# Kernel optimization log

Hardware: AMD Instinct MI355X
Metric: run time of the kernel (lower is better)

## Reference

```python
import jax, jax.numpy as jnp
import numpy as np

NEG_SLOPE = 0.2


def gat_conv(x, src, dst, W, a_src, a_dst, bias, concat, num_nodes):
    # x: [N, F_in]; W: [F_in, H*C]; a_src/a_dst: [H, C]
    H, C = a_src.shape
    h = (x @ W).reshape(num_nodes, H, C)               # [N,H,C]
    alpha_s = jnp.sum(h * a_src[None], axis=-1)        # [N,H]
    alpha_d = jnp.sum(h * a_dst[None], axis=-1)        # [N,H]
    e = jax.nn.leaky_relu(alpha_s[src] + alpha_d[dst], NEG_SLOPE)  # [E,H]
    m = jax.ops.segment_max(e, dst, num_segments=num_nodes)
    m = jnp.where(jnp.isfinite(m), m, 0.0)
    ex = jnp.exp(e - m[dst])
    denom = jax.ops.segment_sum(ex, dst, num_segments=num_nodes)
    alpha = ex / (denom[dst] + 1e-16)                  # scatter-softmax over dst
    msg = h[src] * alpha[:, :, None]                   # [E,H,C]
    out = jax.ops.segment_sum(msg, dst, num_segments=num_nodes)  # [N,H,C]
    if concat:
        out = out.reshape(num_nodes, H * C)
    else:
        out = out.mean(axis=1)
    return out + bias


def setup_inputs() -> dict:
    key = jax.random.key(0)
    ks = jax.random.split(key, 12)
    N, E = 50000, 800000
    num_concat, F_in, hid, H1, H2, n_cls = 2, 128, 64, 4, 1, 16
    x_list = jax.random.normal(ks[0], (num_concat, N, F_in), dtype=jnp.float32)
    edge_index = jax.random.randint(ks[1], (2, E), 0, N, dtype=jnp.int64)
    s = 0.1
    W1 = jax.random.normal(ks[2], (num_concat, F_in, H1 * hid), dtype=jnp.float32) * s
    att_src1 = jax.random.normal(ks[3], (num_concat, H1, hid), dtype=jnp.float32) * s
    att_dst1 = jax.random.normal(ks[4], (num_concat, H1, hid), dtype=jnp.float32) * s
    bias1 = jnp.zeros((num_concat, H1 * hid), dtype=jnp.float32)
    W2 = jax.random.normal(ks[5], (hid * H1 * num_concat, H2 * n_cls), dtype=jnp.float32) * s
    att_src2 = jax.random.normal(ks[6], (H2, n_cls), dtype=jnp.float32) * s
    att_dst2 = jax.random.normal(ks[7], (H2, n_cls), dtype=jnp.float32) * s
    bias2 = jnp.zeros((n_cls,), dtype=jnp.float32)
    return {"x_list": x_list, "edge_index": edge_index,
            "W1": W1, "att_src1": att_src1, "att_dst1": att_dst1, "bias1": bias1,
            "W2": W2, "att_src2": att_src2, "att_dst2": att_dst2, "bias2": bias2}


def reference(x_list, edge_index, W1, att_src1, att_dst1, bias1, W2, att_src2, att_dst2, bias2):
    num_concat, N, _ = x_list.shape
    loop = jnp.arange(N, dtype=edge_index.dtype)
    src = jnp.concatenate([edge_index[0], loop])  # PyG add_self_loops=True
    dst = jnp.concatenate([edge_index[1], loop])
    hidden = [jax.nn.elu(gat_conv(x_list[k], src, dst, W1[k], att_src1[k], att_dst1[k],
                                  bias1[k], True, N))
              for k in range(num_concat)]
    x = jnp.concatenate(hidden, axis=-1)           # [N, hid*H1*num_concat]
    out = gat_conv(x, src, dst, W2, att_src2, att_dst2, bias2, False, N)
    return out
```

## Files before the change

### kernel.cpp

```cpp
#include <hip/hip_runtime.h>

#define LEAKY(v) ((v) >= 0.0f ? (v) : 0.2f * (v))

typedef __attribute__((ext_vector_type(8))) short bf16x8;
typedef __attribute__((ext_vector_type(4))) float f32x4;

__device__ __forceinline__ unsigned short f2bf(float f) {
    unsigned int u = __float_as_uint(f);
    unsigned int r = u + 0x7FFFu + ((u >> 16) & 1u);
    return (unsigned short)(r >> 16);
}
__device__ __forceinline__ float bf2f(unsigned short u) {
    return __uint_as_float(((unsigned int)u) << 16);
}
__device__ __forceinline__ unsigned int pk2(float a, float b) {
    return (unsigned int)f2bf(a) | ((unsigned int)f2bf(b) << 16);
}


__global__ __launch_bounds__(256) void count_deg(const int* ei, int* deg, int E, int Etot) {
    int i = blockIdx.x * 256 + threadIdx.x;
    if (i >= Etot) return;
    int d = (i < E) ? ei[E + i] : (i - E);
    atomicAdd(&deg[d], 1);
}

__global__ __launch_bounds__(512) void scan_block(const int* deg, int* excl, int* bsum, int n) {
    __shared__ int s[512];
    int t = threadIdx.x;
    int i = blockIdx.x * 512 + t;
    int v = (i < n) ? deg[i] : 0;
    s[t] = v;
    __syncthreads();
    for (int d = 1; d < 512; d <<= 1) {
        int x = 0;
        if (t >= d) x = s[t - d];
        __syncthreads();
        if (t >= d) s[t] += x;
        __syncthreads();
    }
    if (i < n) excl[i] = s[t] - v;
    if (t == 511) bsum[blockIdx.x] = s[511];
}

__global__ __launch_bounds__(512) void scan_sums(const int* bsum, int* boff, int nb) {
    __shared__ int s[512];
    int t = threadIdx.x;
    int v = (t < nb) ? bsum[t] : 0;
    s[t] = v;
    __syncthreads();
    for (int d = 1; d < 512; d <<= 1) {
        int x = 0;
        if (t >= d) x = s[t - d];
        __syncthreads();
        if (t >= d) s[t] += x;
        __syncthreads();
    }
    boff[t] = s[t] - v;
}

__global__ __launch_bounds__(256) void finalize_off(int* csr, int* cursor, const int* boff, int n, int etot) {
    int i = blockIdx.x * 256 + threadIdx.x;
    if (i < n) {
        int v = csr[i] + boff[i >> 9];
        csr[i] = v;
        cursor[i] = v;
    }
    if (i == 0) csr[n] = etot;
}

__global__ __launch_bounds__(256) void scatter_edge(const int* ei, int* cursor, int* srcs, int* dsts,
                                                    int E, int Etot) {
    int i = blockIdx.x * 256 + threadIdx.x;
    if (i >= Etot) return;
    int s, d;
    if (i < E) { s = ei[i]; d = ei[E + i]; }
    else       { s = i - E; d = s; }
    int pos = atomicAdd(&cursor[d], 1);
    srcs[pos] = s;
    dsts[pos] = d;
}


__global__ __launch_bounds__(256) void xpack(const float* __restrict__ x, unsigned short* __restrict__ xp,
                                             int nrows) {
    int id = blockIdx.x * 256 + threadIdx.x;
    if (id >= nrows * 16) return;
    int row = id >> 4, q = id & 15;
    const float* src = x + (size_t)row * 128 + q * 8;
    float4 a = *(const float4*)src;
    float4 b = *(const float4*)(src + 4);
    uint4 v;
    v.x = pk2(a.x, a.y); v.y = pk2(a.z, a.w);
    v.z = pk2(b.x, b.y); v.w = pk2(b.z, b.w);
    *(uint4*)(xp + (size_t)row * 128 + ((q ^ (row & 7)) << 3)) = v;
}

__global__ __launch_bounds__(256) void wpack1(const float* __restrict__ W1, unsigned short* __restrict__ wt1) {
    int id = blockIdx.x * 256 + threadIdx.x;
    if (id >= 8192) return;
    int conv = id >> 12, rem = id & 4095;
    int c = rem >> 4, q = rem & 15;
    const float* src = W1 + (size_t)conv * 32768 + (size_t)(q * 8) * 256 + c;
    float w[8];
#pragma unroll
    for (int j = 0; j < 8; ++j) w[j] = src[j * 256];
    uint4 v;
    v.x = pk2(w[0], w[1]); v.y = pk2(w[2], w[3]);
    v.z = pk2(w[4], w[5]); v.w = pk2(w[6], w[7]);
    *(uint4*)(wt1 + (size_t)conv * 32768 + c * 128 + ((q ^ (c & 7)) << 3)) = v;
}

__global__ __launch_bounds__(256) void wpack2(const float* __restrict__ W2, unsigned short* __restrict__ wt2) {
    int id = blockIdx.x * 256 + threadIdx.x;
    if (id >= 1024) return;
    int s = id >> 6, l = id & 63;
    const float* src = W2 + (size_t)(s * 32 + (l >> 4) * 8) * 16 + (l & 15);
    float w[8];
#pragma unroll
    for (int j = 0; j < 8; ++j) w[j] = src[j * 16];
    uint4 v;
    v.x = pk2(w[0], w[1]); v.y = pk2(w[2], w[3]);
    v.z = pk2(w[4], w[5]); v.w = pk2(w[6], w[7]);
    *(uint4*)(wt2 + (size_t)id * 8) = v;
}


__global__ __launch_bounds__(256) void gemm1_mfma(const unsigned short* __restrict__ xp,
                                                  const unsigned short* __restrict__ wt1,
                                                  const float* __restrict__ asw, const float* __restrict__ adw,
                                                  unsigned short* __restrict__ hp,
                                                  float* __restrict__ as1, float* __restrict__ ad1, int N) {
    __shared__ unsigned short As[64 * 128];
    __shared__ unsigned short Ws[256 * 128];
    int conv = blockIdx.y;
    int t = threadIdx.x;
    int w = t >> 6, l = t & 63;

    const uint4* xsrc = (const uint4*)(xp + ((size_t)conv * N + (size_t)blockIdx.x * 64) * 128);
#pragma unroll
    for (int p = 0; p < 4; ++p) {
        int id = p * 256 + t;
        int row = id >> 4;
        int grow = blockIdx.x * 64 + row;
        uint4 v = make_uint4(0, 0, 0, 0);
        if (grow < N) v = xsrc[id];
        *(uint4*)(As + (size_t)id * 8) = v;
    }
    const uint4* wsrc = (const uint4*)(wt1 + (size_t)conv * 32768);
#pragma unroll
    for (int p = 0; p < 16; ++p) {
        int id = p * 256 + t;
        *(uint4*)(Ws + (size_t)id * 8) = wsrc[id];
    }
    __syncthreads();

    f32x4 acc[4][4];
#pragma unroll
    for (int mt = 0; mt < 4; ++mt)
#pragma unroll
        for (int nt = 0; nt < 4; ++nt) acc[mt][nt] = (f32x4){0.f, 0.f, 0.f, 0.f};

    int lr = l & 15, lg = l >> 4;
#pragma unroll
    for (int s = 0; s < 4; ++s) {
        int kq = s * 4 + lg;
        bf16x8 af[4], bf[4];
#pragma unroll
        for (int mt = 0; mt < 4; ++mt) {
            int r = mt * 16 + lr;
            af[mt] = *(const bf16x8*)(As + r * 128 + ((kq ^ (r & 7)) << 3));
        }
#pragma unroll
        for (int nt = 0; nt < 4; ++nt) {
            int c = w * 64 + nt * 16 + lr;
            bf[nt] = *(const bf16x8*)(Ws + c * 128 + ((kq ^ (c & 7)) << 3));
        }
#pragma unroll
        for (int mt = 0; mt < 4; ++mt)
#pragma unroll
            for (int nt = 0; nt < 4; ++nt)
                acc[mt][nt] = __builtin_amdgcn_mfma_f32_16x16x32_bf16(af[mt], bf[nt], acc[mt][nt], 0, 0, 0);
    }

    float aswv[4], adwv[4];
#pragma unroll
    for (int nt = 0; nt < 4; ++nt) {
        aswv[nt] = asw[conv * 256 + w * 64 + nt * 16 + lr];
        adwv[nt] = adw[conv * 256 + w * 64 + nt * 16 + lr];
    }
#pragma unroll
    for (int mt = 0; mt < 4; ++mt) {
#pragma unroll
        for (int i = 0; i < 4; ++i) {
            int grow = blockIdx.x * 64 + mt * 16 + lg * 4 + i;
            bool ok = grow < N;
            float sv = 0.f, dv = 0.f;
#pragma unroll
            for (int nt = 0; nt < 4; ++nt) {
                float hv = acc[mt][nt][i];
                if (ok) hp[(size_t)grow * 512 + (nt * 16 + lr) * 8 + conv * 4 + w] = f2bf(hv);
                sv += hv * aswv[nt];
                dv += hv * adwv[nt];
            }
#pragma unroll
            for (int o = 1; o < 16; o <<= 1) {
                sv += __shfl_xor(sv, o);
                dv += __shfl_xor(dv, o);
            }
            if (lr == 0 && ok) {
                as1[(size_t)conv * N * 4 + (size_t)grow * 4 + w] = sv;
                ad1[(size_t)conv * N * 4 + (size_t)grow * 4 + w] = dv;
            }
        }
    }
}


__global__ __launch_bounds__(256) void edge_w1(const int* __restrict__ srcs, const int* __restrict__ dsts,
                                               const float* __restrict__ as, const float* __restrict__ ad,
                                               float* __restrict__ pw, int Etot, int N4) {
    int e = blockIdx.x * 256 + threadIdx.x;
    if (e >= Etot) return;
    int s = srcs[e], d = dsts[e];
    float4 a0 = *(const float4*)(as + (size_t)s * 4);
    float4 b0 = *(const float4*)(ad + (size_t)d * 4);
    float4 a1 = *(const float4*)(as + N4 + (size_t)s * 4);
    float4 b1 = *(const float4*)(ad + N4 + (size_t)d * 4);
    float4 p0, p1;
    p0.x = __expf(LEAKY(a0.x + b0.x));
    p0.y = __expf(LEAKY(a0.y + b0.y));
    p0.z = __expf(LEAKY(a0.z + b0.z));
    p0.w = __expf(LEAKY(a0.w + b0.w));
    p1.x = __expf(LEAKY(a1.x + b1.x));
    p1.y = __expf(LEAKY(a1.y + b1.y));
    p1.z = __expf(LEAKY(a1.z + b1.z));
    p1.w = __expf(LEAKY(a1.w + b1.w));
    *(float4*)(pw + (size_t)e * 8)     = p0;
    *(float4*)(pw + (size_t)e * 8 + 4) = p1;
}


#define ACC8(g, pa, pb) {                                                      \
    float h0 = __uint_as_float((g).x << 16), h1 = __uint_as_float((g).x & 0xFFFF0000u); \
    float h2v = __uint_as_float((g).y << 16), h3 = __uint_as_float((g).y & 0xFFFF0000u); \
    float h4 = __uint_as_float((g).z << 16), h5 = __uint_as_float((g).z & 0xFFFF0000u); \
    float h6 = __uint_as_float((g).w << 16), h7 = __uint_as_float((g).w & 0xFFFF0000u); \
    den[0] += (pa).x; acc[0] += (pa).x * h0;                                   \
    den[1] += (pa).y; acc[1] += (pa).y * h1;                                   \
    den[2] += (pa).z; acc[2] += (pa).z * h2v;                                  \
    den[3] += (pa).w; acc[3] += (pa).w * h3;                                   \
    den[4] += (pb).x; acc[4] += (pb).x * h4;                                   \
    den[5] += (pb).y; acc[5] += (pb).y * h5;                                   \
    den[6] += (pb).z; acc[6] += (pb).z * h6;                                   \
    den[7] += (pb).w; acc[7] += (pb).w * h7; }

__global__ __launch_bounds__(256) void agg1_both(const unsigned short* __restrict__ hp,
                                                 const float* __restrict__ pw,
                                                 const int* __restrict__ off, const int* __restrict__ srcs,
                                                 const float* __restrict__ b1,
                                                 unsigned short* __restrict__ x2, int N) {
    int n = blockIdx.x * 4 + (threadIdx.x >> 6);
    int lane = threadIdx.x & 63;
    if (n >= N) return;
    int r0 = off[n], r1 = off[n + 1];

    float acc[8] = {0.f, 0.f, 0.f, 0.f, 0.f, 0.f, 0.f, 0.f};
    float den[8] = {0.f, 0.f, 0.f, 0.f, 0.f, 0.f, 0.f, 0.f};

    for (int base = r0; base < r1; base += 64) {
        int cnt = min(64, r1 - base);
        int my = (base + lane < r1) ? srcs[base + lane] : 0;
        int j = 0;
        for (; j + 2 <= cnt; j += 2) {
            int s0 = __shfl(my, j);
            int s1 = __shfl(my, j + 1);
            uint4 g0 = *(const uint4*)(hp + (size_t)s0 * 512 + lane * 8);
            uint4 g1 = *(const uint4*)(hp + (size_t)s1 * 512 + lane * 8);
            float4 pa0 = *(const float4*)(pw + (size_t)(base + j) * 8);
            float4 pb0 = *(const float4*)(pw + (size_t)(base + j) * 8 + 4);
            float4 pa1 = *(const float4*)(pw + (size_t)(base + j + 1) * 8);
            float4 pb1 = *(const float4*)(pw + (size_t)(base + j + 1) * 8 + 4);
            ACC8(g0, pa0, pb0);
            ACC8(g1, pa1, pb1);
        }
        if (j < cnt) {
            int s0 = __shfl(my, j);
            uint4 g0 = *(const uint4*)(hp + (size_t)s0 * 512 + lane * 8);
            float4 pa0 = *(const float4*)(pw + (size_t)(base + j) * 8);
            float4 pb0 = *(const float4*)(pw + (size_t)(base + j) * 8 + 4);
            ACC8(g0, pa0, pb0);
        }
    }

    unsigned short* xo = x2 + (size_t)n * 512;
#pragma unroll
    for (int q = 0; q < 8; ++q) {
        int k = q >> 2, hd = q & 3;
        int ofs = k * 256 + hd * 64 + lane;
        float o = acc[q] / (den[q] + 1e-16f) + b1[ofs];
        o = o > 0.f ? o : (__expf(o) - 1.0f);
        xo[ofs] = f2bf(o);
    }
}


__global__ __launch_bounds__(256) void gemm2_mfma(const unsigned short* __restrict__ x2,
                                                  const unsigned short* __restrict__ wt2,
                                                  const float* __restrict__ asw2, const float* __restrict__ adw2,
                                                  float* __restrict__ h2,
                                                  float* __restrict__ as2, float* __restrict__ ad2, int N) {
    int t = threadIdx.x;
    int w = t >> 6, l = t & 63;
    int rowbase = (blockIdx.x * 4 + w) * 16;
    if (rowbase >= N) return;
    int lr = l & 15, lg = l >> 4;

    f32x4 acc = (f32x4){0.f, 0.f, 0.f, 0.f};
    const unsigned short* ap = x2 + (size_t)(rowbase + lr) * 512 + lg * 8;
#pragma unroll
    for (int s = 0; s < 16; ++s) {
        bf16x8 av = *(const bf16x8*)(ap + s * 32);
        bf16x8 bv = *(const bf16x8*)(wt2 + ((size_t)s * 64 + l) * 8);
        acc = __builtin_amdgcn_mfma_f32_16x16x32_bf16(av, bv, acc, 0, 0, 0);
    }

    float asv = asw2[lr], adv = adw2[lr];
#pragma unroll
    for (int i = 0; i < 4; ++i) {
        int row = rowbase + lg * 4 + i;
        if (row < N) h2[(size_t)row * 16 + lr] = acc[i];
        float sv = acc[i] * asv, dv = acc[i] * adv;
#pragma unroll
        for (int o = 1; o < 16; o <<= 1) {
            sv += __shfl_xor(sv, o);
            dv += __shfl_xor(dv, o);
        }
        if (lr == 0 && row < N) { as2[row] = sv; ad2[row] = dv; }
    }
}


__global__ __launch_bounds__(256) void edge_w2(const int* __restrict__ srcs, const int* __restrict__ dsts,
                                               const float* __restrict__ as2, const float* __restrict__ ad2,
                                               float* __restrict__ p2, int Etot) {
    int e = blockIdx.x * 256 + threadIdx.x;
    if (e >= Etot) return;
    float v = as2[srcs[e]] + ad2[dsts[e]];
    p2[e] = __expf(LEAKY(v));
}


__global__ __launch_bounds__(256) void agg2(const float* __restrict__ h2,
                                            const float* __restrict__ p2,
                                            const int* __restrict__ off, const int* __restrict__ srcs,
                                            const float* __restrict__ bias2, float* __restrict__ out, int N) {
    int n = blockIdx.x * 4 + (threadIdx.x >> 6);
    int lane = threadIdx.x & 63;
    if (n >= N) return;
    int r0 = off[n], r1 = off[n + 1];

    int c = lane & 15, q = lane >> 4;
    float acc = 0.f, denom = 0.f;
    for (int e = r0 + q; e < r1; e += 4) {
        int s = srcs[e];
        float p = p2[e];
        denom += p;
        acc += p * h2[(size_t)s * 16 + c];
    }
    acc += __shfl_xor(acc, 16);     acc += __shfl_xor(acc, 32);
    denom += __shfl_xor(denom, 16); denom += __shfl_xor(denom, 32);
    if (lane < 16) out[(size_t)n * 16 + c] = acc / (denom + 1e-16f) + bias2[c];
}


extern "C" void kernel_launch(void* const* d_in, const int* in_sizes, int n_in,
                              void* d_out, int out_size, void* d_ws, size_t ws_size,
                              hipStream_t stream) {
    const float* x_list = (const float*)d_in[0];
    const int*   ei     = (const int*)d_in[1];
    const float* W1     = (const float*)d_in[2];
    const float* as1w   = (const float*)d_in[3];
    const float* ad1w   = (const float*)d_in[4];
    const float* b1     = (const float*)d_in[5];
    const float* W2     = (const float*)d_in[6];
    const float* as2w   = (const float*)d_in[7];
    const float* ad2w   = (const float*)d_in[8];
    const float* b2     = (const float*)d_in[9];
    float* out = (float*)d_out;

    const int N = in_sizes[0] / 256;
    const int E = in_sizes[1] / 2;
    const int Etot = E + N;
    const int N4 = N * 4;

    char* ws = (char*)d_ws;
    size_t woff = 0;
    auto alloc = [&](size_t bytes) {
        char* p = ws + woff;
        woff = (woff + bytes + 255) & ~(size_t)255;
        return p;
    };
    int*   csr    = (int*)alloc((size_t)(N + 1) * 4);
    int*   cursor = (int*)alloc((size_t)N * 4);
    int*   srcs   = (int*)alloc((size_t)Etot * 4);
    int*   dsts   = (int*)alloc((size_t)Etot * 4);
    int*   bsum   = (int*)alloc(512 * 4);
    int*   boff   = (int*)alloc(512 * 4);
    float* as1    = (float*)alloc((size_t)N4 * 2 * 4);
    float* ad1    = (float*)alloc((size_t)N4 * 2 * 4);
    float* as2    = (float*)alloc((size_t)N * 4);
    float* ad2    = (float*)alloc((size_t)N * 4);
    unsigned short* xp  = (unsigned short*)alloc((size_t)N * 128 * 2 * 2);
    unsigned short* wt1 = (unsigned short*)alloc(2 * 32768 * 2);
    unsigned short* wt2 = (unsigned short*)alloc(16 * 64 * 8 * 2);
    unsigned short* hp  = (unsigned short*)alloc((size_t)N * 512 * 2);
    unsigned short* x2  = (unsigned short*)alloc((size_t)N * 512 * 2);
    float* h2     = (float*)alloc((size_t)N * 16 * 4);
    float* pw     = (float*)alloc((size_t)Etot * 8 * 4);
    float* p2     = (float*)alloc((size_t)Etot * 4);

    hipMemsetAsync(cursor, 0, (size_t)N * 4, stream);
    int gE = (Etot + 255) / 256;
    count_deg<<<gE, 256, 0, stream>>>(ei, cursor, E, Etot);
    int nb = (N + 511) / 512;
    scan_block<<<nb, 512, 0, stream>>>(cursor, csr, bsum, N);
    scan_sums<<<1, 512, 0, stream>>>(bsum, boff, nb);
    finalize_off<<<(N + 255) / 256, 256, 0, stream>>>(csr, cursor, boff, N, Etot);
    scatter_edge<<<gE, 256, 0, stream>>>(ei, cursor, srcs, dsts, E, Etot);

    for (int k = 0; k < 2; ++k)
        xpack<<<(N * 16 + 255) / 256, 256, 0, stream>>>(x_list + (size_t)k * N * 128,
                                                        xp + (size_t)k * N * 128, N);
    wpack1<<<32, 256, 0, stream>>>(W1, wt1);
    wpack2<<<4, 256, 0, stream>>>(W2, wt2);

    gemm1_mfma<<<dim3((N + 63) / 64, 2), 256, 0, stream>>>(xp, wt1, as1w, ad1w, hp, as1, ad1, N);
    edge_w1<<<gE, 256, 0, stream>>>(srcs, dsts, as1, ad1, pw, Etot, N4);
    agg1_both<<<(N + 3) / 4, 256, 0, stream>>>(hp, pw, csr, srcs, b1, x2, N);

    gemm2_mfma<<<(N + 63) / 64, 256, 0, stream>>>(x2, wt2, as2w, ad2w, h2, as2, ad2, N);
    edge_w2<<<gE, 256, 0, stream>>>(srcs, dsts, as2, ad2, p2, Etot);
    agg2<<<(N + 3) / 4, 256, 0, stream>>>(h2, p2, csr, srcs, b2, out, N);
}
```

Before: 354.1 us.

## Fuse x bf16 packing into gemm1, fuse edge_w2 into agg2, unroll agg1

```diff
diff --git a/kernel.cpp b/kernel.cpp
--- a/kernel.cpp
+++ b/kernel.cpp
@@ -10,12 +10,11 @@
     unsigned int r = u + 0x7FFFu + ((u >> 16) & 1u);
     return (unsigned short)(r >> 16);
 }
-__device__ __forceinline__ float bf2f(unsigned short u) {
-    return __uint_as_float(((unsigned int)u) << 16);
-}
 __device__ __forceinline__ unsigned int pk2(float a, float b) {
     return (unsigned int)f2bf(a) | ((unsigned int)f2bf(b) << 16);
 }
+__device__ __forceinline__ float lo16(unsigned int u) { return __uint_as_float(u << 16); }
+__device__ __forceinline__ float hi16(unsigned int u) { return __uint_as_float(u & 0xFFFF0000u); }
 
 
 __global__ __launch_bounds__(256) void count_deg(const int* ei, int* deg, int E, int Etot) {
@@ -82,20 +81,6 @@
 }
 
 
-__global__ __launch_bounds__(256) void xpack(const float* __restrict__ x, unsigned short* __restrict__ xp,
-                                             int nrows) {
-    int id = blockIdx.x * 256 + threadIdx.x;
-    if (id >= nrows * 16) return;
-    int row = id >> 4, q = id & 15;
-    const float* src = x + (size_t)row * 128 + q * 8;
-    float4 a = *(const float4*)src;
-    float4 b = *(const float4*)(src + 4);
-    uint4 v;
-    v.x = pk2(a.x, a.y); v.y = pk2(a.z, a.w);
-    v.z = pk2(b.x, b.y); v.w = pk2(b.z, b.w);
-    *(uint4*)(xp + (size_t)row * 128 + ((q ^ (row & 7)) << 3)) = v;
-}
-
 __global__ __launch_bounds__(256) void wpack1(const float* __restrict__ W1, unsigned short* __restrict__ wt1) {
     int id = blockIdx.x * 256 + threadIdx.x;
     if (id >= 8192) return;
@@ -126,7 +111,7 @@
 }
 
 
-__global__ __launch_bounds__(256) void gemm1_mfma(const unsigned short* __restrict__ xp,
+__global__ __launch_bounds__(256) void gemm1_mfma(const float* __restrict__ x_list,
                                                   const unsigned short* __restrict__ wt1,
                                                   const float* __restrict__ asw, const float* __restrict__ adw,
                                                   unsigned short* __restrict__ hp,
@@ -137,15 +122,21 @@
     int t = threadIdx.x;
     int w = t >> 6, l = t & 63;
 
-    const uint4* xsrc = (const uint4*)(xp + ((size_t)conv * N + (size_t)blockIdx.x * 64) * 128);
+    const float* xg = x_list + (size_t)conv * N * 128;
 #pragma unroll
     for (int p = 0; p < 4; ++p) {
         int id = p * 256 + t;
-        int row = id >> 4;
+        int row = id >> 4, q = id & 15;
         int grow = blockIdx.x * 64 + row;
         uint4 v = make_uint4(0, 0, 0, 0);
-        if (grow < N) v = xsrc[id];
-        *(uint4*)(As + (size_t)id * 8) = v;
+        if (grow < N) {
+            const float* src = xg + (size_t)grow * 128 + q * 8;
+            float4 a = *(const float4*)src;
+            float4 b = *(const float4*)(src + 4);
+            v.x = pk2(a.x, a.y); v.y = pk2(a.z, a.w);
+            v.z = pk2(b.x, b.y); v.w = pk2(b.z, b.w);
+        }
+        *(uint4*)(As + row * 128 + ((q ^ (row & 7)) << 3)) = v;
     }
     const uint4* wsrc = (const uint4*)(wt1 + (size_t)conv * 32768);
 #pragma unroll
@@ -209,8 +200,8 @@
                 dv += __shfl_xor(dv, o);
             }
             if (lr == 0 && ok) {
-                as1[(size_t)conv * N * 4 + (size_t)grow * 4 + w] = sv;
-                ad1[(size_t)conv * N * 4 + (size_t)grow * 4 + w] = dv;
+                as1[((size_t)conv * N + grow) * 4 + w] = sv;
+                ad1[((size_t)conv * N + grow) * 4 + w] = dv;
             }
         }
     }
@@ -242,18 +233,14 @@
 
 
 #define ACC8(g, pa, pb) {                                                      \
-    float h0 = __uint_as_float((g).x << 16), h1 = __uint_as_float((g).x & 0xFFFF0000u); \
-    float h2v = __uint_as_float((g).y << 16), h3 = __uint_as_float((g).y & 0xFFFF0000u); \
-    float h4 = __uint_as_float((g).z << 16), h5 = __uint_as_float((g).z & 0xFFFF0000u); \
-    float h6 = __uint_as_float((g).w << 16), h7 = __uint_as_float((g).w & 0xFFFF0000u); \
-    den[0] += (pa).x; acc[0] += (pa).x * h0;                                   \
-    den[1] += (pa).y; acc[1] += (pa).y * h1;                                   \
-    den[2] += (pa).z; acc[2] += (pa).z * h2v;                                  \
-    den[3] += (pa).w; acc[3] += (pa).w * h3;                                   \
-    den[4] += (pb).x; acc[4] += (pb).x * h4;                                   \
-    den[5] += (pb).y; acc[5] += (pb).y * h5;                                   \
-    den[6] += (pb).z; acc[6] += (pb).z * h6;                                   \
-    den[7] += (pb).w; acc[7] += (pb).w * h7; }
+    den[0] += (pa).x; acc[0] += (pa).x * lo16((g).x);                          \
+    den[1] += (pa).y; acc[1] += (pa).y * hi16((g).x);                          \
+    den[2] += (pa).z; acc[2] += (pa).z * lo16((g).y);                          \
+    den[3] += (pa).w; acc[3] += (pa).w * hi16((g).y);                          \
+    den[4] += (pb).x; acc[4] += (pb).x * lo16((g).z);                          \
+    den[5] += (pb).y; acc[5] += (pb).y * hi16((g).z);                          \
+    den[6] += (pb).z; acc[6] += (pb).z * lo16((g).w);                          \
+    den[7] += (pb).w; acc[7] += (pb).w * hi16((g).w); }
 
 __global__ __launch_bounds__(256) void agg1_both(const unsigned short* __restrict__ hp,
                                                  const float* __restrict__ pw,
@@ -270,25 +257,35 @@
 
     for (int base = r0; base < r1; base += 64) {
         int cnt = min(64, r1 - base);
-        int my = (base + lane < r1) ? srcs[base + lane] : 0;
+        int my = (base + lane < r1) ? __builtin_nontemporal_load(srcs + base + lane) : 0;
         int j = 0;
-        for (; j + 2 <= cnt; j += 2) {
+        for (; j + 4 <= cnt; j += 4) {
             int s0 = __shfl(my, j);
             int s1 = __shfl(my, j + 1);
+            int s2 = __shfl(my, j + 2);
+            int s3 = __shfl(my, j + 3);
             uint4 g0 = *(const uint4*)(hp + (size_t)s0 * 512 + lane * 8);
             uint4 g1 = *(const uint4*)(hp + (size_t)s1 * 512 + lane * 8);
-            float4 pa0 = *(const float4*)(pw + (size_t)(base + j) * 8);
-            float4 pb0 = *(const float4*)(pw + (size_t)(base + j) * 8 + 4);
-            float4 pa1 = *(const float4*)(pw + (size_t)(base + j + 1) * 8);
-            float4 pb1 = *(const float4*)(pw + (size_t)(base + j + 1) * 8 + 4);
+            uint4 g2 = *(const uint4*)(hp + (size_t)s2 * 512 + lane * 8);
+            uint4 g3 = *(const uint4*)(hp + (size_t)s3 * 512 + lane * 8);
+            f32x4 pa0 = __builtin_nontemporal_load((const f32x4*)(pw + (size_t)(base + j) * 8));
+            f32x4 pb0 = __builtin_nontemporal_load((const f32x4*)(pw + (size_t)(base + j) * 8 + 4));
+            f32x4 pa1 = __builtin_nontemporal_load((const f32x4*)(pw + (size_t)(base + j + 1) * 8));
+            f32x4 pb1 = __builtin_nontemporal_load((const f32x4*)(pw + (size_t)(base + j + 1) * 8 + 4));
+            f32x4 pa2 = __builtin_nontemporal_load((const f32x4*)(pw + (size_t)(base + j + 2) * 8));
+            f32x4 pb2 = __builtin_nontemporal_load((const f32x4*)(pw + (size_t)(base + j + 2) * 8 + 4));
+            f32x4 pa3 = __builtin_nontemporal_load((const f32x4*)(pw + (size_t)(base + j + 3) * 8));
+            f32x4 pb3 = __builtin_nontemporal_load((const f32x4*)(pw + (size_t)(base + j + 3) * 8 + 4));
             ACC8(g0, pa0, pb0);
             ACC8(g1, pa1, pb1);
-        }
-        if (j < cnt) {
+            ACC8(g2, pa2, pb2);
+            ACC8(g3, pa3, pb3);
+        }
+        for (; j < cnt; ++j) {
             int s0 = __shfl(my, j);
             uint4 g0 = *(const uint4*)(hp + (size_t)s0 * 512 + lane * 8);
-            float4 pa0 = *(const float4*)(pw + (size_t)(base + j) * 8);
-            float4 pb0 = *(const float4*)(pw + (size_t)(base + j) * 8 + 4);
+            f32x4 pa0 = __builtin_nontemporal_load((const f32x4*)(pw + (size_t)(base + j) * 8));
+            f32x4 pb0 = __builtin_nontemporal_load((const f32x4*)(pw + (size_t)(base + j) * 8 + 4));
             ACC8(g0, pa0, pb0);
         }
     }
@@ -341,36 +338,46 @@
 }
 
 
-__global__ __launch_bounds__(256) void edge_w2(const int* __restrict__ srcs, const int* __restrict__ dsts,
-                                               const float* __restrict__ as2, const float* __restrict__ ad2,
-                                               float* __restrict__ p2, int Etot) {
-    int e = blockIdx.x * 256 + threadIdx.x;
-    if (e >= Etot) return;
-    float v = as2[srcs[e]] + ad2[dsts[e]];
-    p2[e] = __expf(LEAKY(v));
-}
-
-
 __global__ __launch_bounds__(256) void agg2(const float* __restrict__ h2,
-                                            const float* __restrict__ p2,
+                                            const float* __restrict__ as2, const float* __restrict__ ad2,
                                             const int* __restrict__ off, const int* __restrict__ srcs,
                                             const float* __restrict__ bias2, float* __restrict__ out, int N) {
     int n = blockIdx.x * 4 + (threadIdx.x >> 6);
     int lane = threadIdx.x & 63;
     if (n >= N) return;
     int r0 = off[n], r1 = off[n + 1];
-
-    int c = lane & 15, q = lane >> 4;
-    float acc = 0.f, denom = 0.f;
-    for (int e = r0 + q; e < r1; e += 4) {
-        int s = srcs[e];
-        float p = p2[e];
-        denom += p;
-        acc += p * h2[(size_t)s * 16 + c];
-    }
-    acc += __shfl_xor(acc, 16);     acc += __shfl_xor(acc, 32);
-    denom += __shfl_xor(denom, 16); denom += __shfl_xor(denom, 32);
-    if (lane < 16) out[(size_t)n * 16 + c] = acc / (denom + 1e-16f) + bias2[c];
+    float adn = ad2[n];
+    int cg = lane & 3, eo = lane >> 2;
+
+    float4 acc = make_float4(0.f, 0.f, 0.f, 0.f);
+    float den = 0.f;
+    for (int base = r0; base + eo < r1; base += 16) {
+        int e = base + eo;
+        int s = __builtin_nontemporal_load(srcs + e);
+        float p = __expf(LEAKY(as2[s] + adn));
+        float4 hv = *(const float4*)(h2 + (size_t)s * 16 + cg * 4);
+        den += p;
+        acc.x += p * hv.x; acc.y += p * hv.y;
+        acc.z += p * hv.z; acc.w += p * hv.w;
+    }
+#pragma unroll
+    for (int o = 4; o < 64; o <<= 1) {
+        acc.x += __shfl_xor(acc.x, o);
+        acc.y += __shfl_xor(acc.y, o);
+        acc.z += __shfl_xor(acc.z, o);
+        acc.w += __shfl_xor(acc.w, o);
+        den   += __shfl_xor(den, o);
+    }
+    if (eo == 0) {
+        float inv = 1.f / (den + 1e-16f);
+        float4 b = *(const float4*)(bias2 + cg * 4);
+        float4 o4;
+        o4.x = acc.x * inv + b.x;
+        o4.y = acc.y * inv + b.y;
+        o4.z = acc.z * inv + b.z;
+        o4.w = acc.w * inv + b.w;
+        *(float4*)(out + (size_t)n * 16 + cg * 4) = o4;
+    }
 }
 
 
@@ -411,14 +418,12 @@
     float* ad1    = (float*)alloc((size_t)N4 * 2 * 4);
     float* as2    = (float*)alloc((size_t)N * 4);
     float* ad2    = (float*)alloc((size_t)N * 4);
-    unsigned short* xp  = (unsigned short*)alloc((size_t)N * 128 * 2 * 2);
     unsigned short* wt1 = (unsigned short*)alloc(2 * 32768 * 2);
     unsigned short* wt2 = (unsigned short*)alloc(16 * 64 * 8 * 2);
     unsigned short* hp  = (unsigned short*)alloc((size_t)N * 512 * 2);
     unsigned short* x2  = (unsigned short*)alloc((size_t)N * 512 * 2);
     float* h2     = (float*)alloc((size_t)N * 16 * 4);
     float* pw     = (float*)alloc((size_t)Etot * 8 * 4);
-    float* p2     = (float*)alloc((size_t)Etot * 4);
 
     hipMemsetAsync(cursor, 0, (size_t)N * 4, stream);
     int gE = (Etot + 255) / 256;
@@ -429,17 +434,13 @@
     finalize_off<<<(N + 255) / 256, 256, 0, stream>>>(csr, cursor, boff, N, Etot);
     scatter_edge<<<gE, 256, 0, stream>>>(ei, cursor, srcs, dsts, E, Etot);
 
-    for (int k = 0; k < 2; ++k)
-        xpack<<<(N * 16 + 255) / 256, 256, 0, stream>>>(x_list + (size_t)k * N * 128,
-                                                        xp + (size_t)k * N * 128, N);
     wpack1<<<32, 256, 0, stream>>>(W1, wt1);
     wpack2<<<4, 256, 0, stream>>>(W2, wt2);
 
-    gemm1_mfma<<<dim3((N + 63) / 64, 2), 256, 0, stream>>>(xp, wt1, as1w, ad1w, hp, as1, ad1, N);
+    gemm1_mfma<<<dim3((N + 63) / 64, 2), 256, 0, stream>>>(x_list, wt1, as1w, ad1w, hp, as1, ad1, N);
     edge_w1<<<gE, 256, 0, stream>>>(srcs, dsts, as1, ad1, pw, Etot, N4);
     agg1_both<<<(N + 3) / 4, 256, 0, stream>>>(hp, pw, csr, srcs, b1, x2, N);
 
     gemm2_mfma<<<(N + 63) / 64, 256, 0, stream>>>(x2, wt2, as2w, ad2w, h2, as2, ad2, N);
-    edge_w2<<<gE, 256, 0, stream>>>(srcs, dsts, as2, ad2, p2, Etot);
-    agg2<<<(N + 3) / 4, 256, 0, stream>>>(h2, p2, csr, srcs, b2, out, N);
-}
+    agg2<<<(N + 3) / 4, 256, 0, stream>>>(h2, as2, ad2, csr, srcs, b2, out, N);
+}
```

New measurement: 351.7 us. No clear change (-0.7%).
